# Performance work log

Measured on AMD Instinct MI355X. Metric: run time of the kernel, lower is better.

Reference implementation:

```python
import jax, jax.numpy as jnp
import numpy as np

B = 16384       # num graphs
N = 524288      # num atoms/nodes
E = 1048576     # num edges
D_EMB = 128     # dim_emb (atom embedding dim from mol_encoder)
D_STATE = 64    # dim_state
D_EDGE = 32     # raw edge_attr feature dim
N_STATES = 10   # dim_state_encoding (embedding vocab)


def setup_inputs() -> dict:
    key = jax.random.key(0)
    ks = jax.random.split(key, 11)
    return {
        "edge_attr": jax.random.normal(ks[0], (E, D_EDGE), dtype=jnp.float32),
        "z_mol": jax.random.normal(ks[1], (B, D_EMB), dtype=jnp.float32),
        "z_atom": jax.random.normal(ks[2], (N, D_EMB), dtype=jnp.float32),
        "state_emb": jax.random.normal(ks[3], (N_STATES, D_STATE), dtype=jnp.float32),
        "W1": jax.random.normal(ks[4], (D_EMB + D_STATE, 32), dtype=jnp.float32) * 0.07,
        "b1": jnp.zeros((32,), dtype=jnp.float32),
        "W2": jax.random.normal(ks[5], (32, 1), dtype=jnp.float32) * 0.18,
        "b2": jnp.zeros((1,), dtype=jnp.float32),
        "state": jax.random.randint(ks[6], (B,), 0, N_STATES),
        "edge_index0": jax.random.randint(ks[7], (E,), 0, N),
        "batch": jnp.sort(jax.random.randint(ks[8], (N,), 0, B)),
    }


def reference(edge_attr, z_mol, z_atom, state_emb, W1, b1, W2, b2,
              state, edge_index0, batch):
    # z_state = self.state_encoder(state)                     [B, Ds]
    z_state = state_emb[state]
    # gather per-node state embedding                         [N, Ds]
    z_state_nodes = z_state[batch]
    # edge_attr = cat([edge_attr, z_state[batch[edge_index[0]]]], 1)  [E, De+Ds]
    edge_attr_out = jnp.concatenate([edge_attr, z_state_nodes[edge_index0]], axis=1)
    # attn = fc_attn(cat([z_atom, z_state[batch]], 1))         [N, 1]
    h = jnp.concatenate([z_atom, z_state_nodes], axis=1)
    logits = jax.nn.leaky_relu(h @ W1 + b1, negative_slope=0.01) @ W2 + b2
    # segment softmax over graphs (PyG torch_geometric.utils.softmax)
    seg_max = jax.ops.segment_max(logits, batch, num_segments=B)   # [B, 1]
    ex = jnp.exp(logits - seg_max[batch])
    seg_sum = jax.ops.segment_sum(ex, batch, num_segments=B)       # [B, 1]
    attn = ex / (seg_sum[batch] + 1e-16)
    # z_mol_state = global_add_pool(attn * z_atom, batch)      [B, D_emb]
    z_mol_state = jax.ops.segment_sum(attn * z_atom, batch, num_segments=B)
    # input to spect_decoder (opaque downstream)               [B, 2*D_emb]
    x = jnp.concatenate([z_mol, z_mol_state], axis=1)
    return (x, edge_attr_out)
```

## Files before the change

kernel.cpp:

```cpp
#include <hip/hip_runtime.h>
#include <math.h>

#define B_GRAPHS 16384
#define N_NODES  524288
#define E_EDGES  1048576
#define D_EMB    128
#define D_STATE  64
#define HID      32
#define PADK     136
#define WPB      4
#define NWIN     (N_NODES / 32)

typedef __attribute__((ext_vector_type(8))) short short8;
typedef __attribute__((ext_vector_type(4))) float f32x4;

__device__ __forceinline__ unsigned short f2bf(float f) {
    unsigned int u = __builtin_bit_cast(unsigned int, f);
    u += 0x7fffu + ((u >> 16) & 1u);
    return (unsigned short)(u >> 16);
}
__device__ __forceinline__ float bf2f(unsigned short s) {
    unsigned int u = ((unsigned int)s) << 16;
    return __builtin_bit_cast(float, u);
}

__global__ __launch_bounds__(256) void prep_kernel(
    const int*   __restrict__ batch,
    const float* __restrict__ state_emb, const float* __restrict__ W1,
    const float* __restrict__ b1, const int* __restrict__ state,
    int* __restrict__ offs, float* __restrict__ hb)
{
    const int bid = blockIdx.x, t = threadIdx.x;
    if (bid < 2048) {
        int i = bid * 256 + t;
        int b = batch[i];
        int prev = (i == 0) ? -1 : batch[i - 1];
        for (int x = prev + 1; x <= b; ++x) offs[x] = i;
        if (i == N_NODES - 1)
            for (int x = b + 1; x <= B_GRAPHS; ++x) offs[x] = N_NODES;
    } else {
        int j = t & 31;
        int g = (bid - 2048) * 8 + (t >> 5);
        int st = state[g];
        const float* zs = state_emb + st * D_STATE;
        float acc = b1[j];
        #pragma unroll 8
        for (int k = 0; k < D_STATE; ++k)
            acc += zs[k] * W1[(D_EMB + k) * HID + j];
        hb[g * HID + j] = acc;
    }
}

__global__ __launch_bounds__(256, 4) void window_kernel(
    const float* __restrict__ z_atom,
    const float* __restrict__ W1,
    const float* __restrict__ W2,
    const float* __restrict__ b2,
    const int*   __restrict__ batch,
    const float* __restrict__ hb,
    float*       __restrict__ out_x,
    float*       __restrict__ Sbuf,
    float*       __restrict__ rec_u,
    float*       __restrict__ rec_s,
    int*         __restrict__ rec_id)
{
    __shared__ unsigned short s_zb[WPB][32][PADK];

    const int t    = threadIdx.x;
    const int lane = t & 63;
    const int w    = t >> 6;
    const int l15  = lane & 15;
    const int kc   = lane >> 4;

    short8 wa[2][4];
    #pragma unroll
    for (int jh = 0; jh < 2; ++jh)
        #pragma unroll
        for (int kb = 0; kb < 4; ++kb)
            #pragma unroll
            for (int i = 0; i < 8; ++i) {
                int k = kb * 32 + kc * 8 + i;
                wa[jh][kb][i] = (short)f2bf(W1[k * HID + jh * 16 + l15]);
            }

    const float b2v = b2[0];
    float w2v[2][4];
    #pragma unroll
    for (int jh = 0; jh < 2; ++jh)
        #pragma unroll
        for (int r = 0; r < 4; ++r)
            w2v[jh][r] = W2[16 * jh + 4 * kc + r];

    unsigned short (*zb)[PADK] = s_zb[w];

    const int win = blockIdx.x * WPB + w;
    const int c0  = win * 32;
    int bv = 0;
    if (lane < 32) bv = batch[c0 + lane];

    const int leftN  = (c0 > 0) ? batch[c0 - 1] : -2;
    const int rightN = (c0 + 32 < N_NODES) ? batch[c0 + 32] : -2;

    float4 hbf[2][2];
    #pragma unroll
    for (int nh = 0; nh < 2; ++nh) {
        int bn = __shfl(bv, l15 + 16 * nh);
        hbf[nh][0] = *(const float4*)&hb[(size_t)bn * HID + 4 * kc];
        hbf[nh][1] = *(const float4*)&hb[(size_t)bn * HID + 16 + 4 * kc];
    }

    const f32x4* za4 = (const f32x4*)z_atom + (size_t)c0 * (D_EMB / 4);
    #pragma unroll
    for (int half = 0; half < 2; ++half) {
        f32x4 tmp[8];
        #pragma unroll
        for (int it = 0; it < 8; ++it) {
            int idx = (half * 8 + it) * 64 + lane;
            int n = idx >> 5, c = idx & 31;
            tmp[it] = __builtin_nontemporal_load(&za4[n * (D_EMB / 4) + c]);
        }
        #pragma unroll
        for (int it = 0; it < 8; ++it) {
            int idx = (half * 8 + it) * 64 + lane;
            int n = idx >> 5, c = idx & 31;
            f32x4 v = tmp[it];
            unsigned lo = (unsigned)f2bf(v[0]) | ((unsigned)f2bf(v[1]) << 16);
            unsigned hi = (unsigned)f2bf(v[2]) | ((unsigned)f2bf(v[3]) << 16);
            *(uint2*)&zb[n][c * 4] = make_uint2(lo, hi);
        }
    }

    f32x4 acc[2][2] = {{{0.f,0.f,0.f,0.f},{0.f,0.f,0.f,0.f}},
                       {{0.f,0.f,0.f,0.f},{0.f,0.f,0.f,0.f}}};
    #pragma unroll
    for (int kb = 0; kb < 4; ++kb) {
        short8 q0 = *(const short8*)&zb[l15][kb * 32 + kc * 8];
        short8 q1 = *(const short8*)&zb[16 + l15][kb * 32 + kc * 8];
        acc[0][0] = __builtin_amdgcn_mfma_f32_16x16x32_bf16(wa[0][kb], q0, acc[0][0], 0, 0, 0);
        acc[1][0] = __builtin_amdgcn_mfma_f32_16x16x32_bf16(wa[1][kb], q0, acc[1][0], 0, 0, 0);
        acc[0][1] = __builtin_amdgcn_mfma_f32_16x16x32_bf16(wa[0][kb], q1, acc[0][1], 0, 0, 0);
        acc[1][1] = __builtin_amdgcn_mfma_f32_16x16x32_bf16(wa[1][kb], q1, acc[1][1], 0, 0, 0);
    }

    float pt[2];
    #pragma unroll
    for (int nh = 0; nh < 2; ++nh) {
        float part = 0.f;
        #pragma unroll
        for (int r = 0; r < 4; ++r) {
            float h = acc[0][nh][r] + (&hbf[nh][0].x)[r];
            h = h > 0.f ? h : 0.01f * h;
            part += h * w2v[0][r];
        }
        #pragma unroll
        for (int r = 0; r < 4; ++r) {
            float h = acc[1][nh][r] + (&hbf[nh][1].x)[r];
            h = h > 0.f ? h : 0.01f * h;
            part += h * w2v[1][r];
        }
        part += __shfl_xor(part, 16);
        part += __shfl_xor(part, 32);
        pt[nh] = __expf(part + b2v);
    }

    float u0 = 0.f, u1 = 0.f, ss = 0.f;
    int cur = __shfl(bv, 0);
    int a = 0;
    bool usedL = false, usedR = false;

    #pragma unroll 4
    for (int n = 0; n < 32; ++n) {
        int bn = __shfl(bv, n);
        if (bn != cur) {
            if (a == 0 && leftN == cur) {
                *(float2*)&rec_u[(size_t)(2 * win) * 128 + lane * 2] = make_float2(u0, u1);
                if (lane == 0) { rec_s[2 * win] = ss; rec_id[2 * win] = cur; }
                usedL = true;
            } else {
                *(float2*)&out_x[(size_t)cur * 256 + 128 + lane * 2] = make_float2(u0, u1);
                if (lane == 0) Sbuf[cur] = ss;
            }
            u0 = u1 = ss = 0.f;
            cur = bn; a = n;
        }
        float pn = (n < 16) ? __shfl(pt[0], n) : __shfl(pt[1], n - 16);
        unsigned zz = *(const unsigned*)&zb[n][lane * 2];
        u0 += pn * bf2f((unsigned short)(zz & 0xffffu));
        u1 += pn * bf2f((unsigned short)(zz >> 16));
        ss += pn;
    }
    {
        bool lb = (a == 0) && (leftN == cur);
        bool rb = (rightN == cur);
        if (lb) {
            *(float2*)&rec_u[(size_t)(2 * win) * 128 + lane * 2] = make_float2(u0, u1);
            if (lane == 0) { rec_s[2 * win] = ss; rec_id[2 * win] = cur; }
            usedL = true;
        } else if (rb) {
            *(float2*)&rec_u[(size_t)(2 * win + 1) * 128 + lane * 2] = make_float2(u0, u1);
            if (lane == 0) { rec_s[2 * win + 1] = ss; rec_id[2 * win + 1] = cur; }
            usedR = true;
        } else {
            *(float2*)&out_x[(size_t)cur * 256 + 128 + lane * 2] = make_float2(u0, u1);
            if (lane == 0) Sbuf[cur] = ss;
        }
    }
    if (lane == 0) {
        if (!usedL) rec_id[2 * win] = -1;
        if (!usedR) rec_id[2 * win + 1] = -1;
    }
}

__global__ __launch_bounds__(256) void combine_kernel(
    const float* __restrict__ z_mol,
    const int*   __restrict__ offs,
    const float* __restrict__ Sbuf,
    const float* __restrict__ rec_u,
    const float* __restrict__ rec_s,
    const int*   __restrict__ rec_id,
    float*       __restrict__ out_x)
{
    const int t = threadIdx.x, lane = t & 63, wv = t >> 6;
    const int g = blockIdx.x * 4 + wv;
    const int gs = offs[g], ge = offs[g + 1];

    float2 U = make_float2(0.f, 0.f);
    float  S = 0.f;
    if (ge > gs) {
        int w0 = gs >> 5, w1 = (ge - 1) >> 5;
        if (w0 == w1) {
            U = *(const float2*)&out_x[(size_t)g * 256 + 128 + lane * 2];
            S = Sbuf[g];
        } else {
            for (int wn = w0; wn <= w1; ++wn) {
                #pragma unroll
                for (int sl = 0; sl < 2; ++sl) {
                    int id = rec_id[2 * wn + sl];
                    if (id == g) {
                        float2 r = *(const float2*)&rec_u[(size_t)(2 * wn + sl) * 128 + lane * 2];
                        U.x += r.x; U.y += r.y;
                        S += rec_s[2 * wn + sl];
                    }
                }
            }
        }
    }
    const float inv = 1.f / (S + 1e-16f);
    float2 zm = *(const float2*)&z_mol[(size_t)g * D_EMB + lane * 2];
    *(float2*)&out_x[(size_t)g * 256 + lane * 2] = zm;
    *(float2*)&out_x[(size_t)g * 256 + 128 + lane * 2] = make_float2(U.x * inv, U.y * inv);
}

#define NB_COPY (E_EDGES * 8 / 256)
__global__ __launch_bounds__(256) void edge_kernel(
    const f32x4* __restrict__ edge_attr4,
    const f32x4* __restrict__ state_emb4,
    const int*   __restrict__ state,
    const int*   __restrict__ eidx,
    const int*   __restrict__ batch,
    f32x4*       __restrict__ out4)
{
    const int bid = blockIdx.x, t = threadIdx.x;
    if (bid < NB_COPY) {
        int tid = bid * 256 + t;
        int e = tid >> 3, q = tid & 7;
        f32x4 v = __builtin_nontemporal_load(&edge_attr4[tid]);
        __builtin_nontemporal_store(v, &out4[(size_t)e * 24 + q]);
    } else {
        int tid = (bid - NB_COPY) * 256 + t;
        int e = tid >> 4, q = tid & 15;
        int n = eidx[e];
        int b = batch[n];
        int s = state[b];
        f32x4 v = state_emb4[s * 16 + q];
        __builtin_nontemporal_store(v, &out4[(size_t)e * 24 + 8 + q]);
    }
}

extern "C" void kernel_launch(void* const* d_in, const int* in_sizes, int n_in,
                              void* d_out, int out_size, void* d_ws, size_t ws_size,
                              hipStream_t stream)
{
    const float* edge_attr = (const float*)d_in[0];
    const float* z_mol     = (const float*)d_in[1];
    const float* z_atom    = (const float*)d_in[2];
    const float* state_emb = (const float*)d_in[3];
    const float* W1        = (const float*)d_in[4];
    const float* b1        = (const float*)d_in[5];
    const float* W2        = (const float*)d_in[6];
    const float* b2        = (const float*)d_in[7];
    const int*   state     = (const int*)d_in[8];
    const int*   eidx      = (const int*)d_in[9];
    const int*   batch     = (const int*)d_in[10];

    float* out_x = (float*)d_out;
    float* out_e = out_x + (size_t)B_GRAPHS * 256;

    int*   offs = (int*)d_ws;
    float* hbuf = (float*)((char*)d_ws + 65552);
    float* Sbuf = (float*)((char*)d_ws + 65552 + (size_t)B_GRAPHS * HID * 4);

    float* recbase = out_e + 80000000ull;
    float* rec_u  = recbase;
    float* rec_s  = rec_u + (size_t)NWIN * 2 * 128;
    int*   rec_id = (int*)(rec_s + (size_t)NWIN * 2);

    prep_kernel<<<4096, 256, 0, stream>>>(batch, state_emb, W1, b1, state, offs, hbuf);

    window_kernel<<<NWIN / WPB, 256, 0, stream>>>(
        z_atom, W1, W2, b2, batch, hbuf, out_x, Sbuf, rec_u, rec_s, rec_id);

    combine_kernel<<<B_GRAPHS / 4, 256, 0, stream>>>(
        z_mol, offs, Sbuf, rec_u, rec_s, rec_id, out_x);

    edge_kernel<<<NB_COPY + (E_EDGES * 16 / 256), 256, 0, stream>>>(
        (const f32x4*)edge_attr, (const f32x4*)state_emb,
        state, eidx, batch, (f32x4*)out_e);
}
```

Before: 171.5 us.

## Fuse edge copy into window kernel and merge boundary segments with atomics

Drops the per-window boundary record buffers and the offsets-based combine kernel. Segments that cross a window edge are now accumulated directly into the output with float atomics, after a prep pass zeroes those outputs. The edge-attribute copy and state-gather blocks are appended to the window kernel's grid, so the edge work overlaps with the attention work in a single launch. A simple finalize kernel then normalizes and writes z_mol. The costs are atomic traffic on boundary graphs, a non-deterministic summation order, and an extra zeroing pass.

```diff
diff --git a/kernel.cpp b/kernel.cpp
--- a/kernel.cpp
+++ b/kernel.cpp
@@ -10,6 +10,9 @@
 #define PADK     136
 #define WPB      4
 #define NWIN     (N_NODES / 32)
+#define WIN_BLOCKS (NWIN / WPB)
+#define NB_COPY    (E_EDGES * 8 / 256)
+#define NB_STATE   (E_EDGES * 16 / 256)
 
 typedef __attribute__((ext_vector_type(8))) short short8;
 typedef __attribute__((ext_vector_type(4))) float f32x4;
@@ -25,22 +28,14 @@
 }
 
 __global__ __launch_bounds__(256) void prep_kernel(
-    const int*   __restrict__ batch,
     const float* __restrict__ state_emb, const float* __restrict__ W1,
     const float* __restrict__ b1, const int* __restrict__ state,
-    int* __restrict__ offs, float* __restrict__ hb)
+    float* __restrict__ hb, f32x4* __restrict__ out_x4, f32x4* __restrict__ Sbuf4)
 {
     const int bid = blockIdx.x, t = threadIdx.x;
     if (bid < 2048) {
-        int i = bid * 256 + t;
-        int b = batch[i];
-        int prev = (i == 0) ? -1 : batch[i - 1];
-        for (int x = prev + 1; x <= b; ++x) offs[x] = i;
-        if (i == N_NODES - 1)
-            for (int x = b + 1; x <= B_GRAPHS; ++x) offs[x] = N_NODES;
-    } else {
         int j = t & 31;
-        int g = (bid - 2048) * 8 + (t >> 5);
+        int g = bid * 8 + (t >> 5);
         int st = state[g];
         const float* zs = state_emb + st * D_STATE;
         float acc = b1[j];
@@ -48,10 +43,16 @@
         for (int k = 0; k < D_STATE; ++k)
             acc += zs[k] * W1[(D_EMB + k) * HID + j];
         hb[g * HID + j] = acc;
-    }
-}
-
-__global__ __launch_bounds__(256, 4) void window_kernel(
+    } else {
+        int i = (bid - 2048) * 256 + t;
+        int g = i >> 5, q = i & 31;
+        f32x4 z = {0.f, 0.f, 0.f, 0.f};
+        out_x4[(size_t)g * 64 + 32 + q] = z;
+        if (i < B_GRAPHS / 4) Sbuf4[i] = z;
+    }
+}
+
+__global__ __launch_bounds__(256, 4) void main_kernel(
     const float* __restrict__ z_atom,
     const float* __restrict__ W1,
     const float* __restrict__ W2,
@@ -60,13 +61,35 @@
     const float* __restrict__ hb,
     float*       __restrict__ out_x,
     float*       __restrict__ Sbuf,
-    float*       __restrict__ rec_u,
-    float*       __restrict__ rec_s,
-    int*         __restrict__ rec_id)
+    const f32x4* __restrict__ edge_attr4,
+    const f32x4* __restrict__ state_emb4,
+    const int*   __restrict__ state,
+    const int*   __restrict__ eidx,
+    f32x4*       __restrict__ out_e4)
 {
     __shared__ unsigned short s_zb[WPB][32][PADK];
 
-    const int t    = threadIdx.x;
+    const int bid = blockIdx.x;
+    const int t   = threadIdx.x;
+
+    if (bid >= WIN_BLOCKS) {
+        if (bid < WIN_BLOCKS + NB_COPY) {
+            int tid = (bid - WIN_BLOCKS) * 256 + t;
+            int e = tid >> 3, q = tid & 7;
+            f32x4 v = __builtin_nontemporal_load(&edge_attr4[tid]);
+            __builtin_nontemporal_store(v, &out_e4[(size_t)e * 24 + q]);
+        } else {
+            int tid = (bid - WIN_BLOCKS - NB_COPY) * 256 + t;
+            int e = tid >> 4, q = tid & 15;
+            int n = eidx[e];
+            int b = batch[n];
+            int s = state[b];
+            f32x4 v = state_emb4[s * 16 + q];
+            __builtin_nontemporal_store(v, &out_e4[(size_t)e * 24 + 8 + q]);
+        }
+        return;
+    }
+
     const int lane = t & 63;
     const int w    = t >> 6;
     const int l15  = lane & 15;
@@ -93,7 +116,7 @@
 
     unsigned short (*zb)[PADK] = s_zb[w];
 
-    const int win = blockIdx.x * WPB + w;
+    const int win = bid * WPB + w;
     const int c0  = win * 32;
     int bv = 0;
     if (lane < 32) bv = batch[c0 + lane];
@@ -166,16 +189,15 @@
     float u0 = 0.f, u1 = 0.f, ss = 0.f;
     int cur = __shfl(bv, 0);
     int a = 0;
-    bool usedL = false, usedR = false;
 
     #pragma unroll 4
     for (int n = 0; n < 32; ++n) {
         int bn = __shfl(bv, n);
         if (bn != cur) {
             if (a == 0 && leftN == cur) {
-                *(float2*)&rec_u[(size_t)(2 * win) * 128 + lane * 2] = make_float2(u0, u1);
-                if (lane == 0) { rec_s[2 * win] = ss; rec_id[2 * win] = cur; }
-                usedL = true;
+                atomicAdd(&out_x[(size_t)cur * 256 + 128 + lane * 2], u0);
+                atomicAdd(&out_x[(size_t)cur * 256 + 129 + lane * 2], u1);
+                if (lane == 0) atomicAdd(&Sbuf[cur], ss);
             } else {
                 *(float2*)&out_x[(size_t)cur * 256 + 128 + lane * 2] = make_float2(u0, u1);
                 if (lane == 0) Sbuf[cur] = ss;
@@ -192,89 +214,29 @@
     {
         bool lb = (a == 0) && (leftN == cur);
         bool rb = (rightN == cur);
-        if (lb) {
-            *(float2*)&rec_u[(size_t)(2 * win) * 128 + lane * 2] = make_float2(u0, u1);
-            if (lane == 0) { rec_s[2 * win] = ss; rec_id[2 * win] = cur; }
-            usedL = true;
-        } else if (rb) {
-            *(float2*)&rec_u[(size_t)(2 * win + 1) * 128 + lane * 2] = make_float2(u0, u1);
-            if (lane == 0) { rec_s[2 * win + 1] = ss; rec_id[2 * win + 1] = cur; }
-            usedR = true;
+        if (lb || rb) {
+            atomicAdd(&out_x[(size_t)cur * 256 + 128 + lane * 2], u0);
+            atomicAdd(&out_x[(size_t)cur * 256 + 129 + lane * 2], u1);
+            if (lane == 0) atomicAdd(&Sbuf[cur], ss);
         } else {
             *(float2*)&out_x[(size_t)cur * 256 + 128 + lane * 2] = make_float2(u0, u1);
             if (lane == 0) Sbuf[cur] = ss;
         }
     }
-    if (lane == 0) {
-        if (!usedL) rec_id[2 * win] = -1;
-        if (!usedR) rec_id[2 * win + 1] = -1;
-    }
-}
-
-__global__ __launch_bounds__(256) void combine_kernel(
-    const float* __restrict__ z_mol,
-    const int*   __restrict__ offs,
-    const float* __restrict__ Sbuf,
-    const float* __restrict__ rec_u,
-    const float* __restrict__ rec_s,
-    const int*   __restrict__ rec_id,
-    float*       __restrict__ out_x)
-{
-    const int t = threadIdx.x, lane = t & 63, wv = t >> 6;
-    const int g = blockIdx.x * 4 + wv;
-    const int gs = offs[g], ge = offs[g + 1];
-
-    float2 U = make_float2(0.f, 0.f);
-    float  S = 0.f;
-    if (ge > gs) {
-        int w0 = gs >> 5, w1 = (ge - 1) >> 5;
-        if (w0 == w1) {
-            U = *(const float2*)&out_x[(size_t)g * 256 + 128 + lane * 2];
-            S = Sbuf[g];
-        } else {
-            for (int wn = w0; wn <= w1; ++wn) {
-                #pragma unroll
-                for (int sl = 0; sl < 2; ++sl) {
-                    int id = rec_id[2 * wn + sl];
-                    if (id == g) {
-                        float2 r = *(const float2*)&rec_u[(size_t)(2 * wn + sl) * 128 + lane * 2];
-                        U.x += r.x; U.y += r.y;
-                        S += rec_s[2 * wn + sl];
-                    }
-                }
-            }
-        }
-    }
-    const float inv = 1.f / (S + 1e-16f);
-    float2 zm = *(const float2*)&z_mol[(size_t)g * D_EMB + lane * 2];
-    *(float2*)&out_x[(size_t)g * 256 + lane * 2] = zm;
-    *(float2*)&out_x[(size_t)g * 256 + 128 + lane * 2] = make_float2(U.x * inv, U.y * inv);
-}
-
-#define NB_COPY (E_EDGES * 8 / 256)
-__global__ __launch_bounds__(256) void edge_kernel(
-    const f32x4* __restrict__ edge_attr4,
-    const f32x4* __restrict__ state_emb4,
-    const int*   __restrict__ state,
-    const int*   __restrict__ eidx,
-    const int*   __restrict__ batch,
-    f32x4*       __restrict__ out4)
-{
-    const int bid = blockIdx.x, t = threadIdx.x;
-    if (bid < NB_COPY) {
-        int tid = bid * 256 + t;
-        int e = tid >> 3, q = tid & 7;
-        f32x4 v = __builtin_nontemporal_load(&edge_attr4[tid]);
-        __builtin_nontemporal_store(v, &out4[(size_t)e * 24 + q]);
-    } else {
-        int tid = (bid - NB_COPY) * 256 + t;
-        int e = tid >> 4, q = tid & 15;
-        int n = eidx[e];
-        int b = batch[n];
-        int s = state[b];
-        f32x4 v = state_emb4[s * 16 + q];
-        __builtin_nontemporal_store(v, &out4[(size_t)e * 24 + 8 + q]);
-    }
+}
+
+__global__ __launch_bounds__(256) void finalize_kernel(
+    const float* __restrict__ z_mol, const float* __restrict__ Sbuf,
+    float* __restrict__ out_x)
+{
+    int i = blockIdx.x * 256 + threadIdx.x;
+    int g = i >> 5, q = i & 31;
+    f32x4 zm = *(const f32x4*)&z_mol[(size_t)g * D_EMB + q * 4];
+    *(f32x4*)&out_x[(size_t)g * 256 + q * 4] = zm;
+    float inv = 1.f / (Sbuf[g] + 1e-16f);
+    f32x4 u = *(f32x4*)&out_x[(size_t)g * 256 + 128 + q * 4];
+    u *= inv;
+    *(f32x4*)&out_x[(size_t)g * 256 + 128 + q * 4] = u;
 }
 
 extern "C" void kernel_launch(void* const* d_in, const int* in_sizes, int n_in,
@@ -296,24 +258,16 @@
     float* out_x = (float*)d_out;
     float* out_e = out_x + (size_t)B_GRAPHS * 256;
 
-    int*   offs = (int*)d_ws;
-    float* hbuf = (float*)((char*)d_ws + 65552);
-    float* Sbuf = (float*)((char*)d_ws + 65552 + (size_t)B_GRAPHS * HID * 4);
-
-    float* recbase = out_e + 80000000ull;
-    float* rec_u  = recbase;
-    float* rec_s  = rec_u + (size_t)NWIN * 2 * 128;
-    int*   rec_id = (int*)(rec_s + (size_t)NWIN * 2);
-
-    prep_kernel<<<4096, 256, 0, stream>>>(batch, state_emb, W1, b1, state, offs, hbuf);
-
-    window_kernel<<<NWIN / WPB, 256, 0, stream>>>(
-        z_atom, W1, W2, b2, batch, hbuf, out_x, Sbuf, rec_u, rec_s, rec_id);
-
-    combine_kernel<<<B_GRAPHS / 4, 256, 0, stream>>>(
-        z_mol, offs, Sbuf, rec_u, rec_s, rec_id, out_x);
-
-    edge_kernel<<<NB_COPY + (E_EDGES * 16 / 256), 256, 0, stream>>>(
-        (const f32x4*)edge_attr, (const f32x4*)state_emb,
-        state, eidx, batch, (f32x4*)out_e);
-}
+    float* hbuf = (float*)d_ws;
+    float* Sbuf = (float*)((char*)d_ws + (size_t)B_GRAPHS * HID * 4);
+
+    prep_kernel<<<4096, 256, 0, stream>>>(
+        state_emb, W1, b1, state, hbuf, (f32x4*)out_x, (f32x4*)Sbuf);
+
+    main_kernel<<<WIN_BLOCKS + NB_COPY + NB_STATE, 256, 0, stream>>>(
+        z_atom, W1, W2, b2, batch, hbuf, out_x, Sbuf,
+        (const f32x4*)edge_attr, (const f32x4*)state_emb, state, eidx,
+        (f32x4*)out_e);
+
+    finalize_kernel<<<(B_GRAPHS * 32) / 256, 256, 0, stream>>>(z_mol, Sbuf, out_x);
+}
```

After: 190.4 us. +11.0%, slower.
